# Performance work log

Hardware: AMD Instinct MI355X
Metric: run time of the kernel (lower is better)

The kernel has to match this reference:

```python
import jax, jax.numpy as jnp
import numpy as np

N = 100000   # nodes
E = 1600000  # edges (avg degree 16)
IN = 128     # in_channels
H = 64       # num_hidden -> conv1 out = 2*H = 128
RRELU_SLOPE = (1.0 / 8.0 + 1.0 / 3.0) / 2.0  # F.rrelu eval: mean of (lower, upper)


def setup_inputs() -> dict:
    key = jax.random.key(0)
    k1, k2, k3, k4 = jax.random.split(key, 4)
    x = jax.random.normal(k1, (N, IN), dtype=jnp.float32)
    edge_index = jax.random.randint(k2, (2, E), 0, N, dtype=jnp.int32)
    # Glorot-ish init for the two GCN linear layers (PyG GCNConv has weight + bias)
    W1 = jax.random.normal(k3, (IN, 2 * H), dtype=jnp.float32) * (1.0 / np.sqrt(IN))
    b1 = jnp.zeros((2 * H,), dtype=jnp.float32)
    W2 = jax.random.normal(k4, (2 * H, H), dtype=jnp.float32) * (1.0 / np.sqrt(2 * H))
    b2 = jnp.zeros((H,), dtype=jnp.float32)
    return {"x": x, "edge_index": edge_index, "W1": W1, "b1": b1, "W2": W2, "b2": b2}


def _gcn_conv(x, row, col, norm, W, b, n):
    # PyG GCNConv: transform, gather source nodes, scale by sym norm, scatter-add to targets
    h = x @ W                                   # [N, out]
    msg = h[row] * norm[:, None]                # [E+N, out] gathered messages
    return jax.ops.segment_sum(msg, col, num_segments=n) + b


def reference(x, edge_index, W1, b1, W2, b2):
    n = x.shape[0]
    loops = jnp.arange(n, dtype=edge_index.dtype)
    row = jnp.concatenate([edge_index[0], loops])  # sources (with self-loops)
    col = jnp.concatenate([edge_index[1], loops])  # targets (with self-loops)
    deg = jax.ops.segment_sum(jnp.ones_like(col, dtype=x.dtype), col, num_segments=n)
    dinv = jnp.where(deg > 0, jax.lax.rsqrt(deg), 0.0)
    norm = dinv[row] * dinv[col]                  # deg^{-1/2}[u] * deg^{-1/2}[v]
    h = _gcn_conv(x, row, col, norm, W1, b1, n)
    h = jnp.where(h >= 0, h, RRELU_SLOPE * h)     # rrelu (eval mode)
    return _gcn_conv(h, row, col, norm, W2, b2, n)
```

## Files before the change

kernel.cpp:

```cpp
#include <hip/hip_runtime.h>


#define C_IN   128
#define C_MID  128
#define C_OUT2 64
#define SLOT_CAP 64
#define SORT_SH  9
#define SORT_W   196
#define SORT_CAP 16384
#define P1_EPT   8

typedef __attribute__((ext_vector_type(8))) short short8;
typedef __attribute__((ext_vector_type(4))) float floatx4;
typedef __attribute__((ext_vector_type(2))) float f32x2;

__device__ __constant__ float kSlope = 0.22916666666666666f;

__device__ __forceinline__ unsigned short f2bf(float f) {
    unsigned u = __builtin_bit_cast(unsigned, f);
    u = (u + 0x7fffu + ((u >> 16) & 1u)) >> 16;
    return (unsigned short)u;
}
__device__ __forceinline__ f32x2 bfpair(int x) {
    return (f32x2){__builtin_bit_cast(float, (unsigned)x << 16),
                   __builtin_bit_cast(float, (unsigned)(x & 0xffff0000))};
}

__global__ __launch_bounds__(256) void sort_prep_kernel(
        const int* __restrict__ ei, int2* __restrict__ sorted,
        int* __restrict__ bcur,
        const float* __restrict__ W1, const float* __restrict__ W2,
        ushort* __restrict__ W1T, ushort* __restrict__ W2T,
        int E, int p1b) {
    if (blockIdx.x >= p1b) {
        int t = (blockIdx.x - p1b) * 256 + threadIdx.x;
        if (t < C_MID * C_IN) {
            int nn = t >> 7, k = t & 127;
            W1T[t] = f2bf(W1[k * C_MID + nn]);
        } else {
            int i = t - C_MID * C_IN;
            if (i < C_OUT2 * C_MID) {
                int nn = i >> 7, k = i & 127;
                W2T[i] = f2bf(W2[k * C_OUT2 + nn]);
            }
        }
        return;
    }
    __shared__ int hist[SORT_W], goff[SORT_W], cur[SORT_W];
    const int tid = threadIdx.x;
    for (int i = tid; i < SORT_W; i += 256) { hist[i] = 0; cur[i] = 0; }
    __syncthreads();
    const int base = blockIdx.x * (P1_EPT * 256);
#pragma unroll
    for (int k = 0; k < P1_EPT; ++k) {
        int e = base + k * 256 + tid;
        if (e < E) atomicAdd(&hist[ei[E + e] >> SORT_SH], 1);
    }
    __syncthreads();
    for (int i = tid; i < SORT_W; i += 256)
        if (hist[i]) goff[i] = atomicAdd(&bcur[i], hist[i]);
    __syncthreads();
#pragma unroll
    for (int k = 0; k < P1_EPT; ++k) {
        int e = base + k * 256 + tid;
        if (e < E) {
            int v = ei[E + e], u = ei[e];
            int b = v >> SORT_SH;
            int p = goff[b] + atomicAdd(&cur[b], 1);
            if (p < SORT_CAP) sorted[(size_t)b * SORT_CAP + p] = (int2){u, v};
        }
    }
}

template <int CO, bool ABF>
__device__ __forceinline__ void gemm_body(char* smem, int row0,
        const void* __restrict__ Xv, const ushort* __restrict__ WT,
        ushort* __restrict__ Y, int n) {
    constexpr int LDW = 136;
    constexpr int NT = CO / 16;
    ushort* Ws = (ushort*)smem;
    const int tid = threadIdx.x, wave = tid >> 6, lane = tid & 63;
    const int m = lane & 15, q = lane >> 4;

#pragma unroll
    for (int c = 0; c < CO / 16; ++c) {
        int id = tid + c * 256;
        int r = id >> 4, h8 = id & 15;
        *(int4*)&Ws[r * LDW + h8 * 8] = ((const int4*)(WT + r * C_IN))[h8];
    }
    __syncthreads();

    const int rowA = min(row0 + wave * 16 + m, n - 1);
    floatx4 acc[NT];
#pragma unroll
    for (int c = 0; c < NT; ++c) acc[c] = (floatx4){0.f, 0.f, 0.f, 0.f};

#pragma unroll
    for (int s = 0; s < 4; ++s) {
        short8 af;
        if constexpr (ABF) {
            af = *(const short8*)((const ushort*)Xv + (size_t)rowA * C_IN + s * 32 + q * 8);
        } else {
            const float* xp = (const float*)Xv + (size_t)rowA * C_IN + s * 32 + q * 8;
            float4 a0 = *(const float4*)xp;
            float4 a1 = *(const float4*)(xp + 4);
            union { unsigned short us[8]; short8 v; } t;
            t.us[0] = f2bf(a0.x); t.us[1] = f2bf(a0.y); t.us[2] = f2bf(a0.z); t.us[3] = f2bf(a0.w);
            t.us[4] = f2bf(a1.x); t.us[5] = f2bf(a1.y); t.us[6] = f2bf(a1.z); t.us[7] = f2bf(a1.w);
            af = t.v;
        }
#pragma unroll
        for (int c = 0; c < NT; ++c) {
            short8 bf = *(short8*)&Ws[(c * 16 + m) * LDW + s * 32 + q * 8];
            acc[c] = __builtin_amdgcn_mfma_f32_16x16x32_bf16(af, bf, acc[c], 0, 0, 0);
        }
    }
#pragma unroll
    for (int c = 0; c < NT; ++c)
#pragma unroll
        for (int i = 0; i < 4; ++i) {
            int rr = row0 + wave * 16 + q * 4 + i;
            if (rr < n) Y[(size_t)rr * CO + c * 16 + m] = f2bf(acc[c][i]);
        }
}

__global__ __launch_bounds__(256) void csr_gemm1_kernel(
        const int2* __restrict__ sorted, const int* __restrict__ bcur,
        int* __restrict__ cnt, float* __restrict__ dinv,
        int* __restrict__ slots,
        const float* __restrict__ X, const ushort* __restrict__ W1T,
        ushort* __restrict__ h1, int n) {
    __shared__ __align__(16) char smem[C_MID * 136 * 2];
    if (blockIdx.x < SORT_W) {
        int* lc = (int*)smem;
        const int b = blockIdx.x, tid = threadIdx.x;
        const int base_v = b << SORT_SH;
        for (int i = tid; i < 512; i += 256) lc[i] = 0;
        __syncthreads();
        const int nb = min(bcur[b], SORT_CAP);
        const int2* src = sorted + (size_t)b * SORT_CAP;
        for (int i = tid; i < nb; i += 256) {
            int2 e = src[i];
            int pos = atomicAdd(&lc[e.y - base_v], 1);
            if (pos < SLOT_CAP - 1) slots[(size_t)e.y * SLOT_CAP + pos] = e.x;
        }
        __syncthreads();
        for (int i = tid; i < 512; i += 256) {
            int v = base_v + i;
            if (v < n) {
                int deg = lc[i];
                int st = min(deg, SLOT_CAP - 1);
                slots[(size_t)v * SLOT_CAP + st] = v;
                cnt[v] = st + 1;
                dinv[v] = rsqrtf((float)(deg + 1));
            }
        }
        return;
    }
    gemm_body<C_MID, false>(smem, (blockIdx.x - SORT_W) * 64, X, W1T, h1, n);
}

template <int CO, bool ABF>
__global__ __launch_bounds__(256) void gemm_mfma(const void* __restrict__ Xv,
                                                 const ushort* __restrict__ WT,
                                                 ushort* __restrict__ Y, int n) {
    __shared__ __align__(16) char smem[CO * 136 * 2];
    gemm_body<CO, ABF>(smem, blockIdx.x * 64, Xv, WT, Y, n);
}

template <int C, bool DO_RRELU, bool OUT_BF>
__global__ __launch_bounds__(256) void agg_kernel(const ushort* __restrict__ H,
                                                  const int* __restrict__ slots,
                                                  const int* __restrict__ cnt,
                                                  const float* __restrict__ dinv,
                                                  const float* __restrict__ bias,
                                                  void* __restrict__ outv, int n) {
    constexpr int GS = C / 8;
    constexpr int NG = 64 / GS;
    constexpr int NCH = 24 / NG;
    const int wave = threadIdx.x >> 6, lane = threadIdx.x & 63;
    const int vA = blockIdx.x * 8 + wave * 2;
    if (vA >= n) return;
    const int vB = (vA + 1 < n) ? vA + 1 : vA;

    int rawA = slots[(size_t)vA * SLOT_CAP + lane];
    int rawB = slots[(size_t)vB * SLOT_CAP + lane];
    const int limA = cnt[vA], limB = cnt[vB];
    const float dvA = dinv[vA], dvB = dinv[vB];
    const int uA = min(max(rawA, 0), n - 1);
    const int uB = min(max(rawB, 0), n - 1);
    const float wA_l = dinv[uA] * dvA;
    const float wB_l = dinv[uB] * dvB;
    const int lastA = limA - 1, lastB = limB - 1;

    const int g = lane / GS, s = lane % GS;

    float wwA[NCH], wwB[NCH];
    int4 ddA[NCH], ddB[NCH];
#pragma unroll
    for (int t = 0; t < NCH; ++t) {
        int jj = t * NG + g;
        int cA = jj < lastA ? jj : lastA;
        int cB = jj < lastB ? jj : lastB;
        int usA = __shfl(uA, cA), usB = __shfl(uB, cB);
        float wsA = __shfl(wA_l, cA), wsB = __shfl(wB_l, cB);
        wwA[t] = (jj < limA) ? wsA : 0.f;
        wwB[t] = (jj < limB) ? wsB : 0.f;
        ddA[t] = *(const int4*)(H + (size_t)usA * C + s * 8);
        ddB[t] = *(const int4*)(H + (size_t)usB * C + s * 8);
    }
    __builtin_amdgcn_sched_barrier(0);

    f32x2 accA[4], accB[4];
#pragma unroll
    for (int k = 0; k < 4; ++k) { accA[k] = (f32x2){0.f, 0.f}; accB[k] = (f32x2){0.f, 0.f}; }
#pragma unroll
    for (int t = 0; t < NCH; ++t) {
        accA[0] += bfpair(ddA[t].x) * wwA[t]; accA[1] += bfpair(ddA[t].y) * wwA[t];
        accA[2] += bfpair(ddA[t].z) * wwA[t]; accA[3] += bfpair(ddA[t].w) * wwA[t];
        accB[0] += bfpair(ddB[t].x) * wwB[t]; accB[1] += bfpair(ddB[t].y) * wwB[t];
        accB[2] += bfpair(ddB[t].z) * wwB[t]; accB[3] += bfpair(ddB[t].w) * wwB[t];
    }
    for (int j = 24; j < limA; j += NG) {
        int jj = j + g;
        int c = jj < lastA ? jj : lastA;
        int u = __shfl(uA, c);
        float wv = __shfl(wA_l, c);
        float wgt = (jj < limA) ? wv : 0.f;
        const int4 d = *(const int4*)(H + (size_t)u * C + s * 8);
        accA[0] += bfpair(d.x) * wgt; accA[1] += bfpair(d.y) * wgt;
        accA[2] += bfpair(d.z) * wgt; accA[3] += bfpair(d.w) * wgt;
    }
    for (int j = 24; j < limB; j += NG) {
        int jj = j + g;
        int c = jj < lastB ? jj : lastB;
        int u = __shfl(uB, c);
        float wv = __shfl(wB_l, c);
        float wgt = (jj < limB) ? wv : 0.f;
        const int4 d = *(const int4*)(H + (size_t)u * C + s * 8);
        accB[0] += bfpair(d.x) * wgt; accB[1] += bfpair(d.y) * wgt;
        accB[2] += bfpair(d.z) * wgt; accB[3] += bfpair(d.w) * wgt;
    }

    float a[8], b8[8];
#pragma unroll
    for (int k = 0; k < 4; ++k) {
        a[2 * k] = accA[k].x; a[2 * k + 1] = accA[k].y;
        b8[2 * k] = accB[k].x; b8[2 * k + 1] = accB[k].y;
    }
#pragma unroll
    for (int k = 0; k < 8; ++k)
#pragma unroll
        for (int off = GS; off < 64; off <<= 1) {
            a[k] += __shfl_xor(a[k], off);
            b8[k] += __shfl_xor(b8[k], off);
        }

    if (g < 2) {
        const int v = (g == 0) ? vA : vB;
        float r[8];
#pragma unroll
        for (int k = 0; k < 8; ++k) {
            float t = (g == 0) ? a[k] : b8[k];
            r[k] = t + bias[s * 8 + k];
            if (DO_RRELU) r[k] = (r[k] >= 0.f) ? r[k] : r[k] * kSlope;
        }
        if constexpr (OUT_BF) {
            union { ushort us[8]; int4 v4; } o;
#pragma unroll
            for (int k = 0; k < 8; ++k) o.us[k] = f2bf(r[k]);
            *(int4*)((ushort*)outv + (size_t)v * C + s * 8) = o.v4;
        } else {
            float* op = (float*)outv + (size_t)v * C + s * 8;
            *(float4*)op       = (float4){r[0], r[1], r[2], r[3]};
            *(float4*)(op + 4) = (float4){r[4], r[5], r[6], r[7]};
        }
    }
}

extern "C" void kernel_launch(void* const* d_in, const int* in_sizes, int n_in,
                              void* d_out, int out_size, void* d_ws, size_t ws_size,
                              hipStream_t stream) {
    const float* x  = (const float*)d_in[0];
    const int*   ei = (const int*)d_in[1];
    const float* W1 = (const float*)d_in[2];
    const float* b1 = (const float*)d_in[3];
    const float* W2 = (const float*)d_in[4];
    const float* b2 = (const float*)d_in[5];
    const int n = in_sizes[0] / C_IN;
    const int E = in_sizes[1] / 2;

    char* w = (char*)d_ws;
    auto alloc = [&](size_t bytes) -> char* {
        char* p = w; w += (bytes + 255) & ~(size_t)255; return p;
    };
    int*    cnt    = (int*)alloc((size_t)n * 4);
    float*  dinv   = (float*)alloc((size_t)n * 4);
    int*    slots  = (int*)alloc((size_t)n * SLOT_CAP * 4);
    ushort* h1     = (ushort*)alloc((size_t)n * C_MID * 2);
    ushort* h2     = (ushort*)alloc((size_t)n * C_MID * 2);
    ushort* h3     = h1;
    ushort* W1T    = (ushort*)alloc((size_t)C_MID * C_IN * 2);
    ushort* W2T    = (ushort*)alloc((size_t)C_OUT2 * C_MID * 2);
    int2*   sorted = (int2*)alloc((size_t)SORT_W * SORT_CAP * 8);
    int*    bcur   = (int*)alloc((size_t)SORT_W * 4);

    const int p1b = (E + P1_EPT * 256 - 1) / (P1_EPT * 256);
    const int prep_blocks = (C_MID * C_IN + C_OUT2 * C_MID + 255) / 256;
    const int gemm1_blocks = (n + 63) / 64;

    hipMemsetAsync(bcur, 0, (size_t)SORT_W * 4, stream);
    sort_prep_kernel<<<p1b + prep_blocks, 256, 0, stream>>>(
        ei, sorted, bcur, W1, W2, W1T, W2T, E, p1b);
    csr_gemm1_kernel<<<SORT_W + gemm1_blocks, 256, 0, stream>>>(
        sorted, bcur, cnt, dinv, slots, x, W1T, h1, n);
    agg_kernel<C_MID, true, true><<<(n + 7) / 8, 256, 0, stream>>>(
        h1, slots, cnt, dinv, b1, h2, n);
    gemm_mfma<C_OUT2, true><<<(n + 63) / 64, 256, 0, stream>>>(h2, W2T, h3, n);
    agg_kernel<C_OUT2, false, false><<<(n + 7) / 8, 256, 0, stream>>>(
        h3, slots, cnt, dinv, b2, d_out, n);
}
```

Measured before the change: 267.2 us.

## Fuse second-layer GEMM into first aggregation kernel epilogue via MFMA

The first aggregation kernel now stages its 8 aggregated, rrelu'd bf16 rows in shared memory and multiplies them by W2 with a 16x16x32 bf16 MFMA, writing the 64-wide h3 directly. The separate gemm_mfma launch and the n x 128 bf16 h2 round-trip through global memory go away. The cost is a block-wide sync plus MFMA work in the aggregation kernel. Each 16x16 MFMA tile is only half used, since rows 8-15 of the A operand are never written, and W2T rows are loaded from global memory by every block.

```diff
diff --git a/kernel.cpp b/kernel.cpp
--- a/kernel.cpp
+++ b/kernel.cpp
@@ -160,27 +160,26 @@
     gemm_body<C_MID, false>(smem, (blockIdx.x - SORT_W) * 64, X, W1T, h1, n);
 }
 
-template <int CO, bool ABF>
-__global__ __launch_bounds__(256) void gemm_mfma(const void* __restrict__ Xv,
-                                                 const ushort* __restrict__ WT,
-                                                 ushort* __restrict__ Y, int n) {
-    __shared__ __align__(16) char smem[CO * 136 * 2];
-    gemm_body<CO, ABF>(smem, blockIdx.x * 64, Xv, WT, Y, n);
-}
-
-template <int C, bool DO_RRELU, bool OUT_BF>
+template <int C, bool DO_RRELU, int OUT_MODE>
 __global__ __launch_bounds__(256) void agg_kernel(const ushort* __restrict__ H,
                                                   const int* __restrict__ slots,
                                                   const int* __restrict__ cnt,
                                                   const float* __restrict__ dinv,
                                                   const float* __restrict__ bias,
-                                                  void* __restrict__ outv, int n) {
+                                                  void* __restrict__ outv, int n,
+                                                  const ushort* __restrict__ W2T) {
     constexpr int GS = C / 8;
     constexpr int NG = 64 / GS;
     constexpr int NCH = 24 / NG;
+    __shared__ ushort Hs[OUT_MODE == 2 ? 8 * 136 : 8];
+    __shared__ int    Vs[8];
     const int wave = threadIdx.x >> 6, lane = threadIdx.x & 63;
-    const int vA = blockIdx.x * 8 + wave * 2;
-    if (vA >= n) return;
+    int vA = blockIdx.x * 8 + wave * 2;
+    if constexpr (OUT_MODE == 2) {
+        vA = min(vA, n - 2);
+    } else {
+        if (vA >= n) return;
+    }
     const int vB = (vA + 1 < n) ? vA + 1 : vA;
 
     int rawA = slots[(size_t)vA * SLOT_CAP + lane];
@@ -256,7 +255,37 @@
             b8[k] += __shfl_xor(b8[k], off);
         }
 
-    if (g < 2) {
+    if constexpr (OUT_MODE == 2) {
+        if (g < 2) {
+            const int v = (g == 0) ? vA : vB;
+            union { ushort us[8]; int4 v4; } o;
+#pragma unroll
+            for (int k = 0; k < 8; ++k) {
+                float t = (g == 0) ? a[k] : b8[k];
+                t += bias[s * 8 + k];
+                if (DO_RRELU) t = (t >= 0.f) ? t : t * kSlope;
+                o.us[k] = f2bf(t);
+            }
+            *(int4*)&Hs[(wave * 2 + g) * 136 + s * 8] = o.v4;
+            if (s == 0) Vs[wave * 2 + g] = v;
+        }
+        __syncthreads();
+        const int m2 = lane & 15, q2 = lane >> 4;
+        floatx4 acc2 = (floatx4){0.f, 0.f, 0.f, 0.f};
+#pragma unroll
+        for (int s2 = 0; s2 < 4; ++s2) {
+            short8 af = *(short8*)&Hs[m2 * 136 + s2 * 32 + q2 * 8];
+            short8 bf = *(const short8*)(W2T + (size_t)(wave * 16 + m2) * C_MID + s2 * 32 + q2 * 8);
+            acc2 = __builtin_amdgcn_mfma_f32_16x16x32_bf16(af, bf, acc2, 0, 0, 0);
+        }
+        ushort* Y2 = (ushort*)outv;
+#pragma unroll
+        for (int i = 0; i < 4; ++i) {
+            int node = q2 * 4 + i;
+            if (node < 8)
+                Y2[(size_t)Vs[node] * C_OUT2 + wave * 16 + m2] = f2bf(acc2[i]);
+        }
+    } else if (g < 2) {
         const int v = (g == 0) ? vA : vB;
         float r[8];
 #pragma unroll
@@ -265,16 +294,9 @@
             r[k] = t + bias[s * 8 + k];
             if (DO_RRELU) r[k] = (r[k] >= 0.f) ? r[k] : r[k] * kSlope;
         }
-        if constexpr (OUT_BF) {
-            union { ushort us[8]; int4 v4; } o;
-#pragma unroll
-            for (int k = 0; k < 8; ++k) o.us[k] = f2bf(r[k]);
-            *(int4*)((ushort*)outv + (size_t)v * C + s * 8) = o.v4;
-        } else {
-            float* op = (float*)outv + (size_t)v * C + s * 8;
-            *(float4*)op       = (float4){r[0], r[1], r[2], r[3]};
-            *(float4*)(op + 4) = (float4){r[4], r[5], r[6], r[7]};
-        }
+        float* op = (float*)outv + (size_t)v * C + s * 8;
+        *(float4*)op       = (float4){r[0], r[1], r[2], r[3]};
+        *(float4*)(op + 4) = (float4){r[4], r[5], r[6], r[7]};
     }
 }
 
@@ -298,8 +320,7 @@
     float*  dinv   = (float*)alloc((size_t)n * 4);
     int*    slots  = (int*)alloc((size_t)n * SLOT_CAP * 4);
     ushort* h1     = (ushort*)alloc((size_t)n * C_MID * 2);
-    ushort* h2     = (ushort*)alloc((size_t)n * C_MID * 2);
-    ushort* h3     = h1;
+    ushort* h3     = (ushort*)alloc((size_t)n * C_OUT2 * 2);
     ushort* W1T    = (ushort*)alloc((size_t)C_MID * C_IN * 2);
     ushort* W2T    = (ushort*)alloc((size_t)C_OUT2 * C_MID * 2);
     int2*   sorted = (int2*)alloc((size_t)SORT_W * SORT_CAP * 8);
@@ -314,9 +335,8 @@
         ei, sorted, bcur, W1, W2, W1T, W2T, E, p1b);
     csr_gemm1_kernel<<<SORT_W + gemm1_blocks, 256, 0, stream>>>(
         sorted, bcur, cnt, dinv, slots, x, W1T, h1, n);
-    agg_kernel<C_MID, true, true><<<(n + 7) / 8, 256, 0, stream>>>(
-        h1, slots, cnt, dinv, b1, h2, n);
-    gemm_mfma<C_OUT2, true><<<(n + 63) / 64, 256, 0, stream>>>(h2, W2T, h3, n);
-    agg_kernel<C_OUT2, false, false><<<(n + 7) / 8, 256, 0, stream>>>(
-        h3, slots, cnt, dinv, b2, d_out, n);
-}
+    agg_kernel<C_MID, true, 2><<<(n + 7) / 8, 256, 0, stream>>>(
+        h1, slots, cnt, dinv, b1, h3, n, W2T);
+    agg_kernel<C_OUT2, false, 0><<<(n + 7) / 8, 256, 0, stream>>>(
+        h3, slots, cnt, dinv, b2, d_out, n, nullptr);
+}
```

Measured after the change: 266.1 us. About the same (-0.4%).
